# Kernel optimization log

Hardware: AMD Instinct MI355X
Metric: run time of the kernel (lower is better)

The kernel has to match this reference:

```python
import jax, jax.numpy as jnp
import numpy as np

N_NODES = 50000
N_EDGES = 800000
N_GRAPHS = 8
D_IN, D_HID, D_OUT = 128, 128, 64


def setup_inputs() -> dict:
    key = jax.random.key(0)
    ks = jax.random.split(key, 8)
    x = jax.random.normal(ks[0], (N_NODES, D_IN), jnp.float32)
    src = jax.random.randint(ks[1], (N_EDGES,), 0, N_NODES, dtype=jnp.int32)
    dst = jax.random.randint(ks[2], (N_EDGES,), 0, N_NODES, dtype=jnp.int32)
    graph_id = jnp.sort(jax.random.randint(ks[3], (N_NODES,), 0, N_GRAPHS, dtype=jnp.int32))
    s1 = 1.0 / np.sqrt(D_IN)
    s2 = 1.0 / np.sqrt(D_HID)
    W1 = jax.random.normal(ks[4], (D_IN, D_HID), jnp.float32) * s1
    b1 = jnp.zeros((D_HID,), jnp.float32)
    W2 = jax.random.normal(ks[5], (D_HID, D_HID), jnp.float32) * s2
    b2 = jnp.zeros((D_HID,), jnp.float32)
    Wl = jax.random.normal(ks[6], (D_HID, D_OUT), jnp.float32) * s2
    bl = jnp.zeros((D_OUT,), jnp.float32)
    return dict(x=x, W1=W1, b1=b1, W2=W2, b2=b2, Wl=Wl, bl=bl,
                src=src, dst=dst, graph_id=graph_id)


def _graph_conv(x, W, b, src, dst):
    # DGL GraphConv, norm='both': h' = D_in^{-1/2} A (D_out^{-1/2} x W) + b
    n = x.shape[0]
    ones = jnp.ones((src.shape[0],), x.dtype)
    out_deg = jax.ops.segment_sum(ones, src, num_segments=n)
    in_deg = jax.ops.segment_sum(ones, dst, num_segments=n)
    norm_src = jax.lax.rsqrt(jnp.clip(out_deg, 1.0))  # [N]
    norm_dst = jax.lax.rsqrt(jnp.clip(in_deg, 1.0))   # [N]
    h = (x * norm_src[:, None]) @ W                    # [N, D]
    agg = jax.ops.segment_sum(h[src], dst, num_segments=n)  # gather-scatter SpMM
    return agg * norm_dst[:, None] + b


def reference(x, W1, b1, W2, b2, Wl, bl, src, dst, graph_id):
    h = jax.nn.relu(_graph_conv(x, W1, b1, src, dst))
    h = _graph_conv(h, W2, b2, src, dst)
    # dgl.mean_nodes over batched graph: per-graph mean of node features
    cnt = jax.ops.segment_sum(jnp.ones((x.shape[0],), x.dtype), graph_id,
                              num_segments=N_GRAPHS)
    pooled = jax.ops.segment_sum(h, graph_id, num_segments=N_GRAPHS)
    means = pooled / jnp.clip(cnt, 1.0)[:, None]       # [B, D_HID]
    return means @ Wl + bl                              # [B, D_OUT]
```

## Files before the change

### kernel.cpp

```cpp
#include <hip/hip_runtime.h>
#include <hip/hip_bf16.h>

#define N_NODES 50000
#define N_EDGES 800000
#define N_GRAPHS 8
#define MAXDEG 64
#define NRANGE 4
#define NCHUNK 64
#define RSZ (N_NODES / NRANGE)
#define CHE (N_EDGES / NCHUNK)

typedef __attribute__((ext_vector_type(8))) short short8;
typedef __attribute__((ext_vector_type(4))) float floatx4;
typedef __attribute__((ext_vector_type(2))) float floatx2;

static __device__ __forceinline__ ushort f2b(float f) {
    union { float f; unsigned u; } v; v.f = f;
    return (ushort)((v.u + 0x7FFF + ((v.u >> 16) & 1)) >> 16);
}
static __device__ __forceinline__ float b2f(unsigned u) {
    union { unsigned u; float f; } v; v.u = u << 16;
    return v.f;
}
static __device__ __forceinline__ unsigned char f2q(float f) {
    int p = __builtin_amdgcn_cvt_pk_fp8_f32(f, f, 0, false);
    return (unsigned char)(p & 0xff);
}

__global__ __launch_bounds__(1024) void prep_kernel(
    const int* __restrict__ src, const int* __restrict__ dst,
    const float* __restrict__ W1, const float* __restrict__ W2,
    const int* __restrict__ gid,
    ushort* __restrict__ counts_in, ushort* __restrict__ counts_out,
    ushort* __restrict__ Wt1, ushort* __restrict__ Wt2,
    int* __restrict__ start)
{
    int b = blockIdx.x, t = threadIdx.x;
    if (b < 256) {
        __shared__ unsigned h[RSZ];
        int c = b & (NCHUNK - 1), r = b >> 6;
        int lo = r * RSZ;
        for (int j = t; j < RSZ; j += 1024) h[j] = 0;
        __syncthreads();
        int ebeg = c * CHE, eend = ebeg + CHE;
        for (int i = ebeg + t; i < eend; i += 1024) {
            int s = src[i], d = dst[i];
            unsigned ds = (unsigned)(d - lo);
            if (ds < RSZ) atomicAdd(&h[ds >> 1], 1u << ((ds & 1) * 16));
            unsigned ss = (unsigned)(s - lo);
            if (ss < RSZ) atomicAdd(&h[(RSZ / 2) + (ss >> 1)], 1u << ((ss & 1) * 16));
        }
        __syncthreads();
        unsigned* ci = (unsigned*)(counts_in  + (size_t)c * N_NODES + lo);
        unsigned* co = (unsigned*)(counts_out + (size_t)c * N_NODES + lo);
        for (int j = t; j < RSZ / 2; j += 1024) {
            ci[j] = h[j];
            co[j] = h[(RSZ / 2) + j];
        }
    } else if (b < 272) {
        int i = (b - 256) * 1024 + t;
        int c = i >> 7, k = i & 127;
        Wt1[i] = f2b(W1[k * 128 + c]);
        Wt2[i] = f2b(W2[k * 128 + c]);
    } else {
        int i = (b - 272) * 1024 + t;
        if (i < N_NODES) {
            int g = gid[i];
            int gp = (i == 0) ? -1 : gid[i - 1];
            for (int k = gp + 1; k <= g; ++k) start[k] = i;
            if (i == N_NODES - 1)
                for (int k = g + 1; k <= N_GRAPHS; ++k) start[k] = N_NODES;
        }
    }
}

__global__ __launch_bounds__(256) void scan_kernel(
    const ushort* __restrict__ counts_in, const ushort* __restrict__ counts_out,
    ushort* __restrict__ base, int* __restrict__ in_deg,
    float* __restrict__ ns, float* __restrict__ nd)
{
    int v = blockIdx.x * 256 + threadIdx.x;
    if (v >= N_NODES) return;
    unsigned od = 0;
    #pragma unroll 8
    for (int c = 0; c < NCHUNK; ++c) od += counts_out[(size_t)c * N_NODES + v];
    unsigned run = 0;
    #pragma unroll 8
    for (int c = 0; c < NCHUNK; ++c) {
        base[(size_t)c * N_NODES + v] = (ushort)run;
        run += counts_in[(size_t)c * N_NODES + v];
    }
    in_deg[v] = (int)run;
    ns[v] = rsqrtf(fmaxf((float)od, 1.f));
    nd[v] = rsqrtf(fmaxf((float)run, 1.f));
}

__global__ __launch_bounds__(1024) void scatter_kernel(
    const int* __restrict__ src, const int* __restrict__ dst,
    const ushort* __restrict__ base, ushort* __restrict__ slot)
{
    __shared__ unsigned h[RSZ / 2];
    int t = threadIdx.x;
    int c = blockIdx.x & (NCHUNK - 1), r = blockIdx.x >> 6;
    int lo = r * RSZ;
    const unsigned* bp = (const unsigned*)(base + (size_t)c * N_NODES + lo);
    for (int j = t; j < RSZ / 2; j += 1024) h[j] = bp[j];
    __syncthreads();
    int ebeg = c * CHE, eend = ebeg + CHE;
    for (int i = ebeg + t; i < eend; i += 1024) {
        int d = dst[i];
        unsigned ds = (unsigned)(d - lo);
        if (ds < RSZ) {
            int sh = (ds & 1) * 16;
            unsigned old = atomicAdd(&h[ds >> 1], 1u << sh);
            unsigned pos = (old >> sh) & 0xffff;
            if (pos < MAXDEG) slot[(size_t)d * MAXDEG + pos] = (ushort)src[i];
        }
    }
}

template<int FP32_IN>
__global__ __launch_bounds__(256, 2) void mfma_gemm_kernel(
    const void* __restrict__ Xv, const float* __restrict__ scale,
    const ushort* __restrict__ Wt, unsigned char* __restrict__ Y, int n)
{
    int t = threadIdx.x;
    int wv = t >> 6, lane = t & 63;
    int m = lane & 15, q = lane >> 4;
    short8 B[8][4];
    #pragma unroll
    for (int cb = 0; cb < 8; ++cb)
        #pragma unroll
        for (int kb = 0; kb < 4; ++kb)
            B[cb][kb] = *(const short8*)&Wt[(size_t)(cb * 16 + m) * 128 + kb * 32 + q * 8];

    int ntile = n >> 4;
    int gw = blockIdx.x * 4 + wv;
    for (int tile = gw; tile < ntile; tile += 2048) {
        int row = tile * 16 + m;
        short8 a[4];
        if (FP32_IN) {
            const float* X = (const float*)Xv;
            float s = scale[row];
            #pragma unroll
            for (int kb = 0; kb < 4; ++kb) {
                const float* p = X + (size_t)row * 128 + kb * 32 + q * 8;
                float4 f0 = *(const float4*)p;
                float4 f1 = *(const float4*)(p + 4);
                short8 av;
                av[0] = (short)f2b(f0.x * s); av[1] = (short)f2b(f0.y * s);
                av[2] = (short)f2b(f0.z * s); av[3] = (short)f2b(f0.w * s);
                av[4] = (short)f2b(f1.x * s); av[5] = (short)f2b(f1.y * s);
                av[6] = (short)f2b(f1.z * s); av[7] = (short)f2b(f1.w * s);
                a[kb] = av;
            }
        } else {
            const ushort* X = (const ushort*)Xv;
            #pragma unroll
            for (int kb = 0; kb < 4; ++kb)
                a[kb] = *(const short8*)(X + (size_t)row * 128 + kb * 32 + q * 8);
        }
        floatx4 acc[8] = {};
        #pragma unroll
        for (int cb = 0; cb < 8; ++cb)
            #pragma unroll
            for (int kb = 0; kb < 4; ++kb)
                acc[cb] = __builtin_amdgcn_mfma_f32_16x16x32_bf16(a[kb], B[cb][kb], acc[cb], 0, 0, 0);
        int rowbase = tile * 16 + q * 4;
        #pragma unroll
        for (int cb = 0; cb < 8; ++cb)
            #pragma unroll
            for (int r = 0; r < 4; ++r)
                Y[(size_t)(rowbase + r) * 128 + cb * 16 + m] = f2q(acc[cb][r]);
    }
}

__global__ __launch_bounds__(256) void spmm_fp8_kernel(
    const unsigned char* __restrict__ H, const int* __restrict__ in_deg,
    const ushort* __restrict__ slot, const float* __restrict__ norm_dst,
    const float* __restrict__ norm_src, const float* __restrict__ bias,
    ushort* __restrict__ Y, int n, int relu_scale)
{
    int w = (blockIdx.x * blockDim.x + threadIdx.x) >> 6;
    int lane = threadIdx.x & 63;
    if (w >= n) return;
    int cnt = min(in_deg[w], MAXDEG);
    const ushort* lst = slot + (size_t)w * MAXDEG;
    int g = lane >> 4;
    int c8 = (lane & 15) * 8;
    int myslot = lst[lane];
    float acc[8] = {};
    for (int e = 0; e < cnt; e += 4) {
        int idx = e + g;
        bool ok = idx < cnt;
        int s = __shfl(myslot, ok ? idx : 0, 64);
        if (ok) {
            uint2 v = *(const uint2*)&H[(size_t)s * 128 + c8];
            floatx2 p01 = __builtin_amdgcn_cvt_pk_f32_fp8((int)v.x, false);
            floatx2 p23 = __builtin_amdgcn_cvt_pk_f32_fp8((int)v.x, true);
            floatx2 p45 = __builtin_amdgcn_cvt_pk_f32_fp8((int)v.y, false);
            floatx2 p67 = __builtin_amdgcn_cvt_pk_f32_fp8((int)v.y, true);
            acc[0] += p01.x; acc[1] += p01.y;
            acc[2] += p23.x; acc[3] += p23.y;
            acc[4] += p45.x; acc[5] += p45.y;
            acc[6] += p67.x; acc[7] += p67.y;
        }
    }
    #pragma unroll
    for (int j = 0; j < 8; ++j) {
        acc[j] += __shfl_xor(acc[j], 16, 64);
        acc[j] += __shfl_xor(acc[j], 32, 64);
    }
    float ndv = norm_dst[w];
    float4 b0 = *(const float4*)&bias[c8];
    float4 b1 = *(const float4*)&bias[c8 + 4];
    float r[8];
    r[0] = acc[0] * ndv + b0.x; r[1] = acc[1] * ndv + b0.y;
    r[2] = acc[2] * ndv + b0.z; r[3] = acc[3] * ndv + b0.w;
    r[4] = acc[4] * ndv + b1.x; r[5] = acc[5] * ndv + b1.y;
    r[6] = acc[6] * ndv + b1.z; r[7] = acc[7] * ndv + b1.w;
    if (relu_scale) {
        float nsv = norm_src[w];
        #pragma unroll
        for (int j = 0; j < 8; ++j) r[j] = fmaxf(r[j], 0.f) * nsv;
    }
    if (lane < 16) {
        uint4 o;
        o.x = (unsigned)f2b(r[0]) | ((unsigned)f2b(r[1]) << 16);
        o.y = (unsigned)f2b(r[2]) | ((unsigned)f2b(r[3]) << 16);
        o.z = (unsigned)f2b(r[4]) | ((unsigned)f2b(r[5]) << 16);
        o.w = (unsigned)f2b(r[6]) | ((unsigned)f2b(r[7]) << 16);
        *(uint4*)&Y[(size_t)w * 128 + c8] = o;
    }
}

__global__ __launch_bounds__(256) void pool_kernel(
    const ushort* __restrict__ H, const int* __restrict__ start,
    float* __restrict__ part)
{
    __shared__ float red[128];
    int t = threadIdx.x;
    int g = blockIdx.x >> 5, j = blockIdx.x & 31;
    int beg0 = start[g], len = start[g + 1] - beg0;
    int sbeg = beg0 + (int)(((long long)len * j) >> 5);
    int send = beg0 + (int)(((long long)len * (j + 1)) >> 5);
    int wv = t >> 6, lane = t & 63;
    int rg = lane >> 4;
    int c8 = (lane & 15) * 8;
    float acc[8] = {};
    for (int v = sbeg + wv * 4 + rg; v < send; v += 16) {
        uint4 u = *(const uint4*)&H[(size_t)v * 128 + c8];
        acc[0] += b2f(u.x & 0xffff); acc[1] += b2f(u.x >> 16);
        acc[2] += b2f(u.y & 0xffff); acc[3] += b2f(u.y >> 16);
        acc[4] += b2f(u.z & 0xffff); acc[5] += b2f(u.z >> 16);
        acc[6] += b2f(u.w & 0xffff); acc[7] += b2f(u.w >> 16);
    }
    #pragma unroll
    for (int k = 0; k < 8; ++k) {
        acc[k] += __shfl_xor(acc[k], 16, 64);
        acc[k] += __shfl_xor(acc[k], 32, 64);
    }
    if (t < 128) red[t] = 0.f;
    __syncthreads();
    if (lane < 16) {
        #pragma unroll
        for (int k = 0; k < 8; ++k) atomicAdd(&red[c8 + k], acc[k]);
    }
    __syncthreads();
    if (t < 128) part[(size_t)blockIdx.x * 128 + t] = red[t];
}

__global__ __launch_bounds__(512) void head_kernel(
    const float* __restrict__ part, const int* __restrict__ start,
    const float* __restrict__ Wl, const float* __restrict__ bl,
    float* __restrict__ out)
{
    __shared__ float means[N_GRAPHS * 128];
    int t = threadIdx.x;
    for (int i = t; i < N_GRAPHS * 128; i += 512) {
        int g = i >> 7, k = i & 127;
        float s = 0.f;
        #pragma unroll 8
        for (int j = 0; j < 32; ++j) s += part[(size_t)(g * 32 + j) * 128 + k];
        float cnt = (float)(start[g + 1] - start[g]);
        means[i] = s / fmaxf(cnt, 1.f);
    }
    __syncthreads();
    int g = t >> 6, c = t & 63;
    float acc = bl[c];
    #pragma unroll 8
    for (int k = 0; k < 128; ++k)
        acc = fmaf(means[g * 128 + k], Wl[k * 64 + c], acc);
    out[g * 64 + c] = acc;
}

extern "C" void kernel_launch(void* const* d_in, const int* in_sizes, int n_in,
                              void* d_out, int out_size, void* d_ws, size_t ws_size,
                              hipStream_t stream) {
    const float* x   = (const float*)d_in[0];
    const float* W1  = (const float*)d_in[1];
    const float* b1  = (const float*)d_in[2];
    const float* W2  = (const float*)d_in[3];
    const float* b2  = (const float*)d_in[4];
    const float* Wl  = (const float*)d_in[5];
    const float* bl  = (const float*)d_in[6];
    const int*   src = (const int*)d_in[7];
    const int*   dst = (const int*)d_in[8];
    const int*   gid = (const int*)d_in[9];

    const int n = N_NODES;

    char* ws = (char*)d_ws;
    size_t off = 0;
    auto alloc = [&](size_t bytes) { size_t o = off; off += (bytes + 255) & ~(size_t)255; return o; };
    unsigned char* hA = (unsigned char*)(ws + alloc((size_t)n * 128));
    ushort* hB        = (ushort*)(ws + alloc((size_t)n * 128 * 2));
    ushort* slot      = (ushort*)(ws + alloc((size_t)n * MAXDEG * 2));
    ushort* counts_in = (ushort*)(ws + alloc((size_t)NCHUNK * n * 2));
    ushort* counts_out= (ushort*)(ws + alloc((size_t)NCHUNK * n * 2));
    ushort* basev     = (ushort*)(ws + alloc((size_t)NCHUNK * n * 2));
    float* norm_src   = (float*) (ws + alloc((size_t)n * 4));
    float* norm_dst   = (float*) (ws + alloc((size_t)n * 4));
    int*   in_deg     = (int*)   (ws + alloc((size_t)n * 4));
    int*   startb     = (int*)   (ws + alloc((size_t)(N_GRAPHS + 1) * 4));
    ushort* Wt1       = (ushort*)(ws + alloc((size_t)128 * 128 * 2));
    ushort* Wt2       = (ushort*)(ws + alloc((size_t)128 * 128 * 2));
    float* part       = (float*) (ws + alloc((size_t)N_GRAPHS * 32 * 128 * 4));

    int spmm_blocks = (n + 3) / 4;

    prep_kernel<<<321, 1024, 0, stream>>>(src, dst, W1, W2, gid,
                                          counts_in, counts_out, Wt1, Wt2, startb);
    scan_kernel<<<(n + 255) / 256, 256, 0, stream>>>(counts_in, counts_out, basev,
                                                     in_deg, norm_src, norm_dst);
    scatter_kernel<<<NRANGE * NCHUNK, 1024, 0, stream>>>(src, dst, basev, slot);
    mfma_gemm_kernel<1><<<512, 256, 0, stream>>>(x, norm_src, Wt1, hA, n);
    spmm_fp8_kernel<<<spmm_blocks, 256, 0, stream>>>(hA, in_deg, slot, norm_dst,
                                                     norm_src, b1, hB, n, 1);
    mfma_gemm_kernel<0><<<512, 256, 0, stream>>>(hB, nullptr, Wt2, hA, n);
    spmm_fp8_kernel<<<spmm_blocks, 256, 0, stream>>>(hA, in_deg, slot, norm_dst,
                                                     nullptr, b2, hB, n, 0);
    pool_kernel<<<N_GRAPHS * 32, 256, 0, stream>>>(hB, startb, part);
    head_kernel<<<1, 512, 0, stream>>>(part, startb, Wl, bl, (float*)d_out);
}
```

Measured before the change: 213.4 us.

## Replace chunked LDS histogram/scan/scatter with global atomic slot build

Removes the three-kernel degree count, prefix scan and chunked scatter, replacing them with a single kernel that uses global atomics on per-node in/out counters to both count degrees and place edges into fixed-width slots. The normalization factors are now computed on the fly from the counters in the GEMM and SpMM kernels, and the GEMM launches one tile per wave with swapped MFMA operands so each lane writes four packed fp8 bytes at once. This trades two launches and large intermediate count arrays for contended global atomics, and makes the order of neighbors within a slot list nondeterministic.

New measurement: 268.9 us. +26.0%, slower.

```diff
diff --git a/kernel.cpp b/kernel.cpp
--- a/kernel.cpp
+++ b/kernel.cpp
@@ -5,10 +5,6 @@
 #define N_EDGES 800000
 #define N_GRAPHS 8
 #define MAXDEG 64
-#define NRANGE 4
-#define NCHUNK 64
-#define RSZ (N_NODES / NRANGE)
-#define CHE (N_EDGES / NCHUNK)
 
 typedef __attribute__((ext_vector_type(8))) short short8;
 typedef __attribute__((ext_vector_type(4))) float floatx4;
@@ -22,48 +18,21 @@
     union { unsigned u; float f; } v; v.u = u << 16;
     return v.f;
 }
-static __device__ __forceinline__ unsigned char f2q(float f) {
-    int p = __builtin_amdgcn_cvt_pk_fp8_f32(f, f, 0, false);
-    return (unsigned char)(p & 0xff);
-}
-
-__global__ __launch_bounds__(1024) void prep_kernel(
-    const int* __restrict__ src, const int* __restrict__ dst,
+
+__global__ __launch_bounds__(1024) void prep0_kernel(
     const float* __restrict__ W1, const float* __restrict__ W2,
-    const int* __restrict__ gid,
-    ushort* __restrict__ counts_in, ushort* __restrict__ counts_out,
+    const int* __restrict__ gid, unsigned* __restrict__ curs,
     ushort* __restrict__ Wt1, ushort* __restrict__ Wt2,
     int* __restrict__ start)
 {
     int b = blockIdx.x, t = threadIdx.x;
-    if (b < 256) {
-        __shared__ unsigned h[RSZ];
-        int c = b & (NCHUNK - 1), r = b >> 6;
-        int lo = r * RSZ;
-        for (int j = t; j < RSZ; j += 1024) h[j] = 0;
-        __syncthreads();
-        int ebeg = c * CHE, eend = ebeg + CHE;
-        for (int i = ebeg + t; i < eend; i += 1024) {
-            int s = src[i], d = dst[i];
-            unsigned ds = (unsigned)(d - lo);
-            if (ds < RSZ) atomicAdd(&h[ds >> 1], 1u << ((ds & 1) * 16));
-            unsigned ss = (unsigned)(s - lo);
-            if (ss < RSZ) atomicAdd(&h[(RSZ / 2) + (ss >> 1)], 1u << ((ss & 1) * 16));
-        }
-        __syncthreads();
-        unsigned* ci = (unsigned*)(counts_in  + (size_t)c * N_NODES + lo);
-        unsigned* co = (unsigned*)(counts_out + (size_t)c * N_NODES + lo);
-        for (int j = t; j < RSZ / 2; j += 1024) {
-            ci[j] = h[j];
-            co[j] = h[(RSZ / 2) + j];
-        }
-    } else if (b < 272) {
-        int i = (b - 256) * 1024 + t;
+    if (b < 16) {
+        int i = b * 1024 + t;
         int c = i >> 7, k = i & 127;
         Wt1[i] = f2b(W1[k * 128 + c]);
         Wt2[i] = f2b(W2[k * 128 + c]);
-    } else {
-        int i = (b - 272) * 1024 + t;
+    } else if (b < 65) {
+        int i = (b - 16) * 1024 + t;
         if (i < N_NODES) {
             int g = gid[i];
             int gp = (i == 0) ? -1 : gid[i - 1];
@@ -71,62 +40,35 @@
             if (i == N_NODES - 1)
                 for (int k = g + 1; k <= N_GRAPHS; ++k) start[k] = N_NODES;
         }
-    }
-}
-
-__global__ __launch_bounds__(256) void scan_kernel(
-    const ushort* __restrict__ counts_in, const ushort* __restrict__ counts_out,
-    ushort* __restrict__ base, int* __restrict__ in_deg,
-    float* __restrict__ ns, float* __restrict__ nd)
-{
-    int v = blockIdx.x * 256 + threadIdx.x;
-    if (v >= N_NODES) return;
-    unsigned od = 0;
-    #pragma unroll 8
-    for (int c = 0; c < NCHUNK; ++c) od += counts_out[(size_t)c * N_NODES + v];
-    unsigned run = 0;
-    #pragma unroll 8
-    for (int c = 0; c < NCHUNK; ++c) {
-        base[(size_t)c * N_NODES + v] = (ushort)run;
-        run += counts_in[(size_t)c * N_NODES + v];
-    }
-    in_deg[v] = (int)run;
-    ns[v] = rsqrtf(fmaxf((float)od, 1.f));
-    nd[v] = rsqrtf(fmaxf((float)run, 1.f));
-}
-
-__global__ __launch_bounds__(1024) void scatter_kernel(
+    } else {
+        int i = (b - 65) * 1024 + t;
+        if (i < (2 * N_NODES) / 4) ((uint4*)curs)[i] = make_uint4(0, 0, 0, 0);
+    }
+}
+
+__global__ __launch_bounds__(256) void edge_scatter_kernel(
     const int* __restrict__ src, const int* __restrict__ dst,
-    const ushort* __restrict__ base, ushort* __restrict__ slot)
-{
-    __shared__ unsigned h[RSZ / 2];
-    int t = threadIdx.x;
-    int c = blockIdx.x & (NCHUNK - 1), r = blockIdx.x >> 6;
-    int lo = r * RSZ;
-    const unsigned* bp = (const unsigned*)(base + (size_t)c * N_NODES + lo);
-    for (int j = t; j < RSZ / 2; j += 1024) h[j] = bp[j];
-    __syncthreads();
-    int ebeg = c * CHE, eend = ebeg + CHE;
-    for (int i = ebeg + t; i < eend; i += 1024) {
-        int d = dst[i];
-        unsigned ds = (unsigned)(d - lo);
-        if (ds < RSZ) {
-            int sh = (ds & 1) * 16;
-            unsigned old = atomicAdd(&h[ds >> 1], 1u << sh);
-            unsigned pos = (old >> sh) & 0xffff;
-            if (pos < MAXDEG) slot[(size_t)d * MAXDEG + pos] = (ushort)src[i];
-        }
-    }
+    unsigned* __restrict__ in_cur, unsigned* __restrict__ out_cur,
+    ushort* __restrict__ slot)
+{
+    int i = blockIdx.x * 256 + threadIdx.x;
+    int s = src[i], d = dst[i];
+    atomicAdd(&out_cur[s], 1u);
+    unsigned pos = atomicAdd(&in_cur[d], 1u);
+    if (pos < MAXDEG) slot[(size_t)d * MAXDEG + pos] = (ushort)s;
 }
 
 template<int FP32_IN>
 __global__ __launch_bounds__(256, 2) void mfma_gemm_kernel(
-    const void* __restrict__ Xv, const float* __restrict__ scale,
-    const ushort* __restrict__ Wt, unsigned char* __restrict__ Y, int n)
+    const void* __restrict__ Xv, const unsigned* __restrict__ odeg,
+    const ushort* __restrict__ Wt, unsigned char* __restrict__ Y)
 {
     int t = threadIdx.x;
     int wv = t >> 6, lane = t & 63;
     int m = lane & 15, q = lane >> 4;
+    int tile = blockIdx.x * 4 + wv;
+    if (tile >= (N_NODES >> 4)) return;
+
     short8 B[8][4];
     #pragma unroll
     for (int cb = 0; cb < 8; ++cb)
@@ -134,57 +76,55 @@
         for (int kb = 0; kb < 4; ++kb)
             B[cb][kb] = *(const short8*)&Wt[(size_t)(cb * 16 + m) * 128 + kb * 32 + q * 8];
 
-    int ntile = n >> 4;
-    int gw = blockIdx.x * 4 + wv;
-    for (int tile = gw; tile < ntile; tile += 2048) {
-        int row = tile * 16 + m;
-        short8 a[4];
-        if (FP32_IN) {
-            const float* X = (const float*)Xv;
-            float s = scale[row];
-            #pragma unroll
-            for (int kb = 0; kb < 4; ++kb) {
-                const float* p = X + (size_t)row * 128 + kb * 32 + q * 8;
-                float4 f0 = *(const float4*)p;
-                float4 f1 = *(const float4*)(p + 4);
-                short8 av;
-                av[0] = (short)f2b(f0.x * s); av[1] = (short)f2b(f0.y * s);
-                av[2] = (short)f2b(f0.z * s); av[3] = (short)f2b(f0.w * s);
-                av[4] = (short)f2b(f1.x * s); av[5] = (short)f2b(f1.y * s);
-                av[6] = (short)f2b(f1.z * s); av[7] = (short)f2b(f1.w * s);
-                a[kb] = av;
-            }
-        } else {
-            const ushort* X = (const ushort*)Xv;
-            #pragma unroll
-            for (int kb = 0; kb < 4; ++kb)
-                a[kb] = *(const short8*)(X + (size_t)row * 128 + kb * 32 + q * 8);
+    int row = tile * 16 + m;
+    short8 a[4];
+    if (FP32_IN) {
+        const float* X = (const float*)Xv;
+        float s = rsqrtf(fmaxf((float)odeg[row], 1.f));
+        #pragma unroll
+        for (int kb = 0; kb < 4; ++kb) {
+            const float* p = X + (size_t)row * 128 + kb * 32 + q * 8;
+            float4 f0 = *(const float4*)p;
+            float4 f1 = *(const float4*)(p + 4);
+            short8 av;
+            av[0] = (short)f2b(f0.x * s); av[1] = (short)f2b(f0.y * s);
+            av[2] = (short)f2b(f0.z * s); av[3] = (short)f2b(f0.w * s);
+            av[4] = (short)f2b(f1.x * s); av[5] = (short)f2b(f1.y * s);
+            av[6] = (short)f2b(f1.z * s); av[7] = (short)f2b(f1.w * s);
+            a[kb] = av;
         }
-        floatx4 acc[8] = {};
-        #pragma unroll
-        for (int cb = 0; cb < 8; ++cb)
-            #pragma unroll
-            for (int kb = 0; kb < 4; ++kb)
-                acc[cb] = __builtin_amdgcn_mfma_f32_16x16x32_bf16(a[kb], B[cb][kb], acc[cb], 0, 0, 0);
-        int rowbase = tile * 16 + q * 4;
-        #pragma unroll
-        for (int cb = 0; cb < 8; ++cb)
-            #pragma unroll
-            for (int r = 0; r < 4; ++r)
-                Y[(size_t)(rowbase + r) * 128 + cb * 16 + m] = f2q(acc[cb][r]);
+    } else {
+        const ushort* X = (const ushort*)Xv;
+        #pragma unroll
+        for (int kb = 0; kb < 4; ++kb)
+            a[kb] = *(const short8*)(X + (size_t)row * 128 + kb * 32 + q * 8);
+    }
+    floatx4 acc[8] = {};
+    #pragma unroll
+    for (int cb = 0; cb < 8; ++cb)
+        #pragma unroll
+        for (int kb = 0; kb < 4; ++kb)
+            acc[cb] = __builtin_amdgcn_mfma_f32_16x16x32_bf16(B[cb][kb], a[kb], acc[cb], 0, 0, 0);
+
+    unsigned char* yr = Y + (size_t)row * 128;
+    #pragma unroll
+    for (int cb = 0; cb < 8; ++cb) {
+        int lo = __builtin_amdgcn_cvt_pk_fp8_f32(acc[cb][0], acc[cb][1], 0, false);
+        int pk = __builtin_amdgcn_cvt_pk_fp8_f32(acc[cb][2], acc[cb][3], lo, true);
+        *(unsigned*)(yr + cb * 16 + q * 4) = (unsigned)pk;
     }
 }
 
 __global__ __launch_bounds__(256) void spmm_fp8_kernel(
-    const unsigned char* __restrict__ H, const int* __restrict__ in_deg,
-    const ushort* __restrict__ slot, const float* __restrict__ norm_dst,
-    const float* __restrict__ norm_src, const float* __restrict__ bias,
-    ushort* __restrict__ Y, int n, int relu_scale)
+    const unsigned char* __restrict__ H, const unsigned* __restrict__ in_cur,
+    const unsigned* __restrict__ out_cur, const ushort* __restrict__ slot,
+    const float* __restrict__ bias, ushort* __restrict__ Y, int relu_scale)
 {
     int w = (blockIdx.x * blockDim.x + threadIdx.x) >> 6;
     int lane = threadIdx.x & 63;
-    if (w >= n) return;
-    int cnt = min(in_deg[w], MAXDEG);
+    if (w >= N_NODES) return;
+    int dg = (int)in_cur[w];
+    int cnt = min(dg, MAXDEG);
     const ushort* lst = slot + (size_t)w * MAXDEG;
     int g = lane >> 4;
     int c8 = (lane & 15) * 8;
@@ -211,7 +151,7 @@
         acc[j] += __shfl_xor(acc[j], 16, 64);
         acc[j] += __shfl_xor(acc[j], 32, 64);
     }
-    float ndv = norm_dst[w];
+    float ndv = rsqrtf(fmaxf((float)dg, 1.f));
     float4 b0 = *(const float4*)&bias[c8];
     float4 b1 = *(const float4*)&bias[c8 + 4];
     float r[8];
@@ -220,7 +160,7 @@
     r[4] = acc[4] * ndv + b1.x; r[5] = acc[5] * ndv + b1.y;
     r[6] = acc[6] * ndv + b1.z; r[7] = acc[7] * ndv + b1.w;
     if (relu_scale) {
-        float nsv = norm_src[w];
+        float nsv = rsqrtf(fmaxf((float)out_cur[w], 1.f));
         #pragma unroll
         for (int j = 0; j < 8; ++j) r[j] = fmaxf(r[j], 0.f) * nsv;
     }
@@ -316,30 +256,24 @@
     unsigned char* hA = (unsigned char*)(ws + alloc((size_t)n * 128));
     ushort* hB        = (ushort*)(ws + alloc((size_t)n * 128 * 2));
     ushort* slot      = (ushort*)(ws + alloc((size_t)n * MAXDEG * 2));
-    ushort* counts_in = (ushort*)(ws + alloc((size_t)NCHUNK * n * 2));
-    ushort* counts_out= (ushort*)(ws + alloc((size_t)NCHUNK * n * 2));
-    ushort* basev     = (ushort*)(ws + alloc((size_t)NCHUNK * n * 2));
-    float* norm_src   = (float*) (ws + alloc((size_t)n * 4));
-    float* norm_dst   = (float*) (ws + alloc((size_t)n * 4));
-    int*   in_deg     = (int*)   (ws + alloc((size_t)n * 4));
+    unsigned* curs    = (unsigned*)(ws + alloc((size_t)2 * n * 4));
     int*   startb     = (int*)   (ws + alloc((size_t)(N_GRAPHS + 1) * 4));
     ushort* Wt1       = (ushort*)(ws + alloc((size_t)128 * 128 * 2));
     ushort* Wt2       = (ushort*)(ws + alloc((size_t)128 * 128 * 2));
     float* part       = (float*) (ws + alloc((size_t)N_GRAPHS * 32 * 128 * 4));
 
+    unsigned* in_cur  = curs;
+    unsigned* out_cur = curs + n;
+
     int spmm_blocks = (n + 3) / 4;
-
-    prep_kernel<<<321, 1024, 0, stream>>>(src, dst, W1, W2, gid,
-                                          counts_in, counts_out, Wt1, Wt2, startb);
-    scan_kernel<<<(n + 255) / 256, 256, 0, stream>>>(counts_in, counts_out, basev,
-                                                     in_deg, norm_src, norm_dst);
-    scatter_kernel<<<NRANGE * NCHUNK, 1024, 0, stream>>>(src, dst, basev, slot);
-    mfma_gemm_kernel<1><<<512, 256, 0, stream>>>(x, norm_src, Wt1, hA, n);
-    spmm_fp8_kernel<<<spmm_blocks, 256, 0, stream>>>(hA, in_deg, slot, norm_dst,
-                                                     norm_src, b1, hB, n, 1);
-    mfma_gemm_kernel<0><<<512, 256, 0, stream>>>(hB, nullptr, Wt2, hA, n);
-    spmm_fp8_kernel<<<spmm_blocks, 256, 0, stream>>>(hA, in_deg, slot, norm_dst,
-                                                     nullptr, b2, hB, n, 0);
+    int gemm_blocks = ((n >> 4) + 3) / 4;
+
+    prep0_kernel<<<90, 1024, 0, stream>>>(W1, W2, gid, curs, Wt1, Wt2, startb);
+    edge_scatter_kernel<<<N_EDGES / 256, 256, 0, stream>>>(src, dst, in_cur, out_cur, slot);
+    mfma_gemm_kernel<1><<<gemm_blocks, 256, 0, stream>>>(x, out_cur, Wt1, hA);
+    spmm_fp8_kernel<<<spmm_blocks, 256, 0, stream>>>(hA, in_cur, out_cur, slot, b1, hB, 1);
+    mfma_gemm_kernel<0><<<gemm_blocks, 256, 0, stream>>>(hB, out_cur, Wt2, hA);
+    spmm_fp8_kernel<<<spmm_blocks, 256, 0, stream>>>(hA, in_cur, out_cur, slot, b2, hB, 0);
     pool_kernel<<<N_GRAPHS * 32, 256, 0, stream>>>(hB, startb, part);
     head_kernel<<<1, 512, 0, stream>>>(part, startb, Wl, bl, (float*)d_out);
 }
```

## Pad neighbor lists with zero sentinel row, unroll SpMM, transpose MFMA for packed stores

Applied to the files above, without the earlier changes.

Neighbor slot lists are pre-filled with 0xFFFF, and a zeroed sentinel row 65535 is added to the hA buffer. The SpMM loop can then process 8 edges per iteration without bounds checks, since padded slots read zeros. The GEMM swaps its MFMA operands so each lane holds four consecutive output columns and writes them as one packed 4-byte fp8 store. It also launches one wave per tile instead of using a grid-stride loop. The cost is an extra 6.4 MB slot fill in the prep kernel and wasted loads on padded edges.

Measured after the change: 218.6 us. 2.4% more time.

```diff
diff --git a/kernel.cpp b/kernel.cpp
--- a/kernel.cpp
+++ b/kernel.cpp
@@ -9,6 +9,7 @@
 #define NCHUNK 64
 #define RSZ (N_NODES / NRANGE)
 #define CHE (N_EDGES / NCHUNK)
+#define SENT_ROW 65535
 
 typedef __attribute__((ext_vector_type(8))) short short8;
 typedef __attribute__((ext_vector_type(4))) float floatx4;
@@ -33,7 +34,8 @@
     const int* __restrict__ gid,
     ushort* __restrict__ counts_in, ushort* __restrict__ counts_out,
     ushort* __restrict__ Wt1, ushort* __restrict__ Wt2,
-    int* __restrict__ start)
+    int* __restrict__ start,
+    unsigned char* __restrict__ hA, uint4* __restrict__ slot_fill)
 {
     int b = blockIdx.x, t = threadIdx.x;
     if (b < 256) {
@@ -62,7 +64,9 @@
         int c = i >> 7, k = i & 127;
         Wt1[i] = f2b(W1[k * 128 + c]);
         Wt2[i] = f2b(W2[k * 128 + c]);
-    } else {
+        if (b == 256 && t < 32)
+            ((unsigned*)(hA + (size_t)SENT_ROW * 128))[t] = 0u;
+    } else if (b < 321) {
         int i = (b - 272) * 1024 + t;
         if (i < N_NODES) {
             int g = gid[i];
@@ -71,6 +75,10 @@
             if (i == N_NODES - 1)
                 for (int k = g + 1; k <= N_GRAPHS; ++k) start[k] = N_NODES;
         }
+    } else {
+        int i = (b - 321) * 1024 + t;
+        if (i < (N_NODES * MAXDEG * 2) / 16)
+            slot_fill[i] = make_uint4(0xFFFFFFFFu, 0xFFFFFFFFu, 0xFFFFFFFFu, 0xFFFFFFFFu);
     }
 }
 
@@ -122,11 +130,14 @@
 template<int FP32_IN>
 __global__ __launch_bounds__(256, 2) void mfma_gemm_kernel(
     const void* __restrict__ Xv, const float* __restrict__ scale,
-    const ushort* __restrict__ Wt, unsigned char* __restrict__ Y, int n)
+    const ushort* __restrict__ Wt, unsigned char* __restrict__ Y)
 {
     int t = threadIdx.x;
     int wv = t >> 6, lane = t & 63;
     int m = lane & 15, q = lane >> 4;
+    int tile = blockIdx.x * 4 + wv;
+    if (tile >= (N_NODES >> 4)) return;
+
     short8 B[8][4];
     #pragma unroll
     for (int cb = 0; cb < 8; ++cb)
@@ -134,44 +145,42 @@
         for (int kb = 0; kb < 4; ++kb)
             B[cb][kb] = *(const short8*)&Wt[(size_t)(cb * 16 + m) * 128 + kb * 32 + q * 8];
 
-    int ntile = n >> 4;
-    int gw = blockIdx.x * 4 + wv;
-    for (int tile = gw; tile < ntile; tile += 2048) {
-        int row = tile * 16 + m;
-        short8 a[4];
-        if (FP32_IN) {
-            const float* X = (const float*)Xv;
-            float s = scale[row];
-            #pragma unroll
-            for (int kb = 0; kb < 4; ++kb) {
-                const float* p = X + (size_t)row * 128 + kb * 32 + q * 8;
-                float4 f0 = *(const float4*)p;
-                float4 f1 = *(const float4*)(p + 4);
-                short8 av;
-                av[0] = (short)f2b(f0.x * s); av[1] = (short)f2b(f0.y * s);
-                av[2] = (short)f2b(f0.z * s); av[3] = (short)f2b(f0.w * s);
-                av[4] = (short)f2b(f1.x * s); av[5] = (short)f2b(f1.y * s);
-                av[6] = (short)f2b(f1.z * s); av[7] = (short)f2b(f1.w * s);
-                a[kb] = av;
-            }
-        } else {
-            const ushort* X = (const ushort*)Xv;
-            #pragma unroll
-            for (int kb = 0; kb < 4; ++kb)
-                a[kb] = *(const short8*)(X + (size_t)row * 128 + kb * 32 + q * 8);
-        }
-        floatx4 acc[8] = {};
-        #pragma unroll
-        for (int cb = 0; cb < 8; ++cb)
-            #pragma unroll
-            for (int kb = 0; kb < 4; ++kb)
-                acc[cb] = __builtin_amdgcn_mfma_f32_16x16x32_bf16(a[kb], B[cb][kb], acc[cb], 0, 0, 0);
-        int rowbase = tile * 16 + q * 4;
-        #pragma unroll
-        for (int cb = 0; cb < 8; ++cb)
-            #pragma unroll
-            for (int r = 0; r < 4; ++r)
-                Y[(size_t)(rowbase + r) * 128 + cb * 16 + m] = f2q(acc[cb][r]);
+    int row = tile * 16 + m;
+    short8 a[4];
+    if (FP32_IN) {
+        const float* X = (const float*)Xv;
+        float s = scale[row];
+        #pragma unroll
+        for (int kb = 0; kb < 4; ++kb) {
+            const float* p = X + (size_t)row * 128 + kb * 32 + q * 8;
+            float4 f0 = *(const float4*)p;
+            float4 f1 = *(const float4*)(p + 4);
+            short8 av;
+            av[0] = (short)f2b(f0.x * s); av[1] = (short)f2b(f0.y * s);
+            av[2] = (short)f2b(f0.z * s); av[3] = (short)f2b(f0.w * s);
+            av[4] = (short)f2b(f1.x * s); av[5] = (short)f2b(f1.y * s);
+            av[6] = (short)f2b(f1.z * s); av[7] = (short)f2b(f1.w * s);
+            a[kb] = av;
+        }
+    } else {
+        const ushort* X = (const ushort*)Xv;
+        #pragma unroll
+        for (int kb = 0; kb < 4; ++kb)
+            a[kb] = *(const short8*)(X + (size_t)row * 128 + kb * 32 + q * 8);
+    }
+    floatx4 acc[8] = {};
+    #pragma unroll
+    for (int cb = 0; cb < 8; ++cb)
+        #pragma unroll
+        for (int kb = 0; kb < 4; ++kb)
+            acc[cb] = __builtin_amdgcn_mfma_f32_16x16x32_bf16(B[cb][kb], a[kb], acc[cb], 0, 0, 0);
+
+    unsigned char* yr = Y + (size_t)row * 128;
+    #pragma unroll
+    for (int cb = 0; cb < 8; ++cb) {
+        int lo = __builtin_amdgcn_cvt_pk_fp8_f32(acc[cb][0], acc[cb][1], 0, false);
+        int pk = __builtin_amdgcn_cvt_pk_fp8_f32(acc[cb][2], acc[cb][3], lo, true);
+        *(unsigned*)(yr + cb * 16 + q * 4) = (unsigned)pk;
     }
 }
 
@@ -179,32 +188,34 @@
     const unsigned char* __restrict__ H, const int* __restrict__ in_deg,
     const ushort* __restrict__ slot, const float* __restrict__ norm_dst,
     const float* __restrict__ norm_src, const float* __restrict__ bias,
-    ushort* __restrict__ Y, int n, int relu_scale)
+    ushort* __restrict__ Y, int relu_scale)
 {
     int w = (blockIdx.x * blockDim.x + threadIdx.x) >> 6;
     int lane = threadIdx.x & 63;
-    if (w >= n) return;
+    if (w >= N_NODES) return;
     int cnt = min(in_deg[w], MAXDEG);
     const ushort* lst = slot + (size_t)w * MAXDEG;
     int g = lane >> 4;
     int c8 = (lane & 15) * 8;
     int myslot = lst[lane];
     float acc[8] = {};
-    for (int e = 0; e < cnt; e += 4) {
-        int idx = e + g;
-        bool ok = idx < cnt;
-        int s = __shfl(myslot, ok ? idx : 0, 64);
-        if (ok) {
-            uint2 v = *(const uint2*)&H[(size_t)s * 128 + c8];
-            floatx2 p01 = __builtin_amdgcn_cvt_pk_f32_fp8((int)v.x, false);
-            floatx2 p23 = __builtin_amdgcn_cvt_pk_f32_fp8((int)v.x, true);
-            floatx2 p45 = __builtin_amdgcn_cvt_pk_f32_fp8((int)v.y, false);
-            floatx2 p67 = __builtin_amdgcn_cvt_pk_f32_fp8((int)v.y, true);
-            acc[0] += p01.x; acc[1] += p01.y;
-            acc[2] += p23.x; acc[3] += p23.y;
-            acc[4] += p45.x; acc[5] += p45.y;
-            acc[6] += p67.x; acc[7] += p67.y;
-        }
+    for (int e = 0; e < cnt; e += 8) {
+        int s0 = __shfl(myslot, e + g, 64);
+        int s1 = __shfl(myslot, e + 4 + g, 64);
+        uint2 v0 = *(const uint2*)&H[(size_t)s0 * 128 + c8];
+        uint2 v1 = *(const uint2*)&H[(size_t)s1 * 128 + c8];
+        floatx2 a01 = __builtin_amdgcn_cvt_pk_f32_fp8((int)v0.x, false);
+        floatx2 a23 = __builtin_amdgcn_cvt_pk_f32_fp8((int)v0.x, true);
+        floatx2 a45 = __builtin_amdgcn_cvt_pk_f32_fp8((int)v0.y, false);
+        floatx2 a67 = __builtin_amdgcn_cvt_pk_f32_fp8((int)v0.y, true);
+        floatx2 b01 = __builtin_amdgcn_cvt_pk_f32_fp8((int)v1.x, false);
+        floatx2 b23 = __builtin_amdgcn_cvt_pk_f32_fp8((int)v1.x, true);
+        floatx2 b45 = __builtin_amdgcn_cvt_pk_f32_fp8((int)v1.y, false);
+        floatx2 b67 = __builtin_amdgcn_cvt_pk_f32_fp8((int)v1.y, true);
+        acc[0] += a01.x + b01.x; acc[1] += a01.y + b01.y;
+        acc[2] += a23.x + b23.x; acc[3] += a23.y + b23.y;
+        acc[4] += a45.x + b45.x; acc[5] += a45.y + b45.y;
+        acc[6] += a67.x + b67.x; acc[7] += a67.y + b67.y;
     }
     #pragma unroll
     for (int j = 0; j < 8; ++j) {
@@ -313,7 +324,7 @@
     char* ws = (char*)d_ws;
     size_t off = 0;
     auto alloc = [&](size_t bytes) { size_t o = off; off += (bytes + 255) & ~(size_t)255; return o; };
-    unsigned char* hA = (unsigned char*)(ws + alloc((size_t)n * 128));
+    unsigned char* hA = (unsigned char*)(ws + alloc((size_t)65536 * 128));
     ushort* hB        = (ushort*)(ws + alloc((size_t)n * 128 * 2));
     ushort* slot      = (ushort*)(ws + alloc((size_t)n * MAXDEG * 2));
     ushort* counts_in = (ushort*)(ws + alloc((size_t)NCHUNK * n * 2));
@@ -328,18 +339,21 @@
     float* part       = (float*) (ws + alloc((size_t)N_GRAPHS * 32 * 128 * 4));
 
     int spmm_blocks = (n + 3) / 4;
-
-    prep_kernel<<<321, 1024, 0, stream>>>(src, dst, W1, W2, gid,
-                                          counts_in, counts_out, Wt1, Wt2, startb);
+    int gemm_blocks = ((n >> 4) + 3) / 4;
+    int fill_blocks = ((N_NODES * MAXDEG * 2) / 16 + 1023) / 1024;
+
+    prep_kernel<<<321 + fill_blocks, 1024, 0, stream>>>(
+        src, dst, W1, W2, gid, counts_in, counts_out, Wt1, Wt2, startb,
+        hA, (uint4*)slot);
     scan_kernel<<<(n + 255) / 256, 256, 0, stream>>>(counts_in, counts_out, basev,
                                                      in_deg, norm_src, norm_dst);
     scatter_kernel<<<NRANGE * NCHUNK, 1024, 0, stream>>>(src, dst, basev, slot);
-    mfma_gemm_kernel<1><<<512, 256, 0, stream>>>(x, norm_src, Wt1, hA, n);
+    mfma_gemm_kernel<1><<<gemm_blocks, 256, 0, stream>>>(x, norm_src, Wt1, hA);
     spmm_fp8_kernel<<<spmm_blocks, 256, 0, stream>>>(hA, in_deg, slot, norm_dst,
-                                                     norm_src, b1, hB, n, 1);
-    mfma_gemm_kernel<0><<<512, 256, 0, stream>>>(hB, nullptr, Wt2, hA, n);
+                                                     norm_src, b1, hB, 1);
+    mfma_gemm_kernel<0><<<gemm_blocks, 256, 0, stream>>>(hB, nullptr, Wt2, hA);
     spmm_fp8_kernel<<<spmm_blocks, 256, 0, stream>>>(hA, in_deg, slot, norm_dst,
-                                                     nullptr, b2, hB, n, 0);
+                                                     nullptr, b2, hB, 0);
     pool_kernel<<<N_GRAPHS * 32, 256, 0, stream>>>(hB, startb, part);
     head_kernel<<<1, 512, 0, stream>>>(part, startb, Wl, bl, (float*)d_out);
 }
```

## Transpose MFMA operands for packed fp8 stores and launch one tile per wave

Applied to the files above, without the earlier changes.

Swaps the A/B operands of the bf16 MFMA so each lane holds four consecutive output columns of one row. This lets the epilogue pack them into a single 32-bit fp8 store per column block instead of 32 scattered byte stores. The GEMM now launches one wave per 16-row tile rather than using a grid-stride loop over 512 blocks. The SpMM gains an occupancy hint of 8 blocks per CU, and n is replaced by the compile-time node count. The tradeoff is that every wave reloads the full weight fragment into registers, adding redundant weight loads.

New measurement: 228.6 us. +7.1%, slower.

```diff
diff --git a/kernel.cpp b/kernel.cpp
--- a/kernel.cpp
+++ b/kernel.cpp
@@ -21,10 +21,6 @@
 static __device__ __forceinline__ float b2f(unsigned u) {
     union { unsigned u; float f; } v; v.u = u << 16;
     return v.f;
-}
-static __device__ __forceinline__ unsigned char f2q(float f) {
-    int p = __builtin_amdgcn_cvt_pk_fp8_f32(f, f, 0, false);
-    return (unsigned char)(p & 0xff);
 }
 
 __global__ __launch_bounds__(1024) void prep_kernel(
@@ -122,11 +118,14 @@
 template<int FP32_IN>
 __global__ __launch_bounds__(256, 2) void mfma_gemm_kernel(
     const void* __restrict__ Xv, const float* __restrict__ scale,
-    const ushort* __restrict__ Wt, unsigned char* __restrict__ Y, int n)
+    const ushort* __restrict__ Wt, unsigned char* __restrict__ Y)
 {
     int t = threadIdx.x;
     int wv = t >> 6, lane = t & 63;
     int m = lane & 15, q = lane >> 4;
+    int tile = blockIdx.x * 4 + wv;
+    if (tile >= (N_NODES >> 4)) return;
+
     short8 B[8][4];
     #pragma unroll
     for (int cb = 0; cb < 8; ++cb)
@@ -134,56 +133,54 @@
         for (int kb = 0; kb < 4; ++kb)
             B[cb][kb] = *(const short8*)&Wt[(size_t)(cb * 16 + m) * 128 + kb * 32 + q * 8];
 
-    int ntile = n >> 4;
-    int gw = blockIdx.x * 4 + wv;
-    for (int tile = gw; tile < ntile; tile += 2048) {
-        int row = tile * 16 + m;
-        short8 a[4];
-        if (FP32_IN) {
-            const float* X = (const float*)Xv;
-            float s = scale[row];
-            #pragma unroll
-            for (int kb = 0; kb < 4; ++kb) {
-                const float* p = X + (size_t)row * 128 + kb * 32 + q * 8;
-                float4 f0 = *(const float4*)p;
-                float4 f1 = *(const float4*)(p + 4);
-                short8 av;
-                av[0] = (short)f2b(f0.x * s); av[1] = (short)f2b(f0.y * s);
-                av[2] = (short)f2b(f0.z * s); av[3] = (short)f2b(f0.w * s);
-                av[4] = (short)f2b(f1.x * s); av[5] = (short)f2b(f1.y * s);
-                av[6] = (short)f2b(f1.z * s); av[7] = (short)f2b(f1.w * s);
-                a[kb] = av;
-            }
-        } else {
-            const ushort* X = (const ushort*)Xv;
-            #pragma unroll
-            for (int kb = 0; kb < 4; ++kb)
-                a[kb] = *(const short8*)(X + (size_t)row * 128 + kb * 32 + q * 8);
-        }
-        floatx4 acc[8] = {};
-        #pragma unroll
-        for (int cb = 0; cb < 8; ++cb)
-            #pragma unroll
-            for (int kb = 0; kb < 4; ++kb)
-                acc[cb] = __builtin_amdgcn_mfma_f32_16x16x32_bf16(a[kb], B[cb][kb], acc[cb], 0, 0, 0);
-        int rowbase = tile * 16 + q * 4;
-        #pragma unroll
-        for (int cb = 0; cb < 8; ++cb)
-            #pragma unroll
-            for (int r = 0; r < 4; ++r)
-                Y[(size_t)(rowbase + r) * 128 + cb * 16 + m] = f2q(acc[cb][r]);
-    }
-}
-
-__global__ __launch_bounds__(256) void spmm_fp8_kernel(
+    int row = tile * 16 + m;
+    short8 a[4];
+    if (FP32_IN) {
+        const float* X = (const float*)Xv;
+        float s = scale[row];
+        #pragma unroll
+        for (int kb = 0; kb < 4; ++kb) {
+            const float* p = X + (size_t)row * 128 + kb * 32 + q * 8;
+            float4 f0 = *(const float4*)p;
+            float4 f1 = *(const float4*)(p + 4);
+            short8 av;
+            av[0] = (short)f2b(f0.x * s); av[1] = (short)f2b(f0.y * s);
+            av[2] = (short)f2b(f0.z * s); av[3] = (short)f2b(f0.w * s);
+            av[4] = (short)f2b(f1.x * s); av[5] = (short)f2b(f1.y * s);
+            av[6] = (short)f2b(f1.z * s); av[7] = (short)f2b(f1.w * s);
+            a[kb] = av;
+        }
+    } else {
+        const ushort* X = (const ushort*)Xv;
+        #pragma unroll
+        for (int kb = 0; kb < 4; ++kb)
+            a[kb] = *(const short8*)(X + (size_t)row * 128 + kb * 32 + q * 8);
+    }
+    floatx4 acc[8] = {};
+    #pragma unroll
+    for (int cb = 0; cb < 8; ++cb)
+        #pragma unroll
+        for (int kb = 0; kb < 4; ++kb)
+            acc[cb] = __builtin_amdgcn_mfma_f32_16x16x32_bf16(B[cb][kb], a[kb], acc[cb], 0, 0, 0);
+
+    unsigned char* yr = Y + (size_t)row * 128;
+    #pragma unroll
+    for (int cb = 0; cb < 8; ++cb) {
+        int lo = __builtin_amdgcn_cvt_pk_fp8_f32(acc[cb][0], acc[cb][1], 0, false);
+        int pk = __builtin_amdgcn_cvt_pk_fp8_f32(acc[cb][2], acc[cb][3], lo, true);
+        *(unsigned*)(yr + cb * 16 + q * 4) = (unsigned)pk;
+    }
+}
+
+__global__ __launch_bounds__(256, 8) void spmm_fp8_kernel(
     const unsigned char* __restrict__ H, const int* __restrict__ in_deg,
     const ushort* __restrict__ slot, const float* __restrict__ norm_dst,
     const float* __restrict__ norm_src, const float* __restrict__ bias,
-    ushort* __restrict__ Y, int n, int relu_scale)
+    ushort* __restrict__ Y, int relu_scale)
 {
     int w = (blockIdx.x * blockDim.x + threadIdx.x) >> 6;
     int lane = threadIdx.x & 63;
-    if (w >= n) return;
+    if (w >= N_NODES) return;
     int cnt = min(in_deg[w], MAXDEG);
     const ushort* lst = slot + (size_t)w * MAXDEG;
     int g = lane >> 4;
@@ -328,18 +325,19 @@
     float* part       = (float*) (ws + alloc((size_t)N_GRAPHS * 32 * 128 * 4));
 
     int spmm_blocks = (n + 3) / 4;
+    int gemm_blocks = ((n >> 4) + 3) / 4;
 
     prep_kernel<<<321, 1024, 0, stream>>>(src, dst, W1, W2, gid,
                                           counts_in, counts_out, Wt1, Wt2, startb);
     scan_kernel<<<(n + 255) / 256, 256, 0, stream>>>(counts_in, counts_out, basev,
                                                      in_deg, norm_src, norm_dst);
     scatter_kernel<<<NRANGE * NCHUNK, 1024, 0, stream>>>(src, dst, basev, slot);
-    mfma_gemm_kernel<1><<<512, 256, 0, stream>>>(x, norm_src, Wt1, hA, n);
+    mfma_gemm_kernel<1><<<gemm_blocks, 256, 0, stream>>>(x, norm_src, Wt1, hA);
     spmm_fp8_kernel<<<spmm_blocks, 256, 0, stream>>>(hA, in_deg, slot, norm_dst,
-                                                     norm_src, b1, hB, n, 1);
-    mfma_gemm_kernel<0><<<512, 256, 0, stream>>>(hB, nullptr, Wt2, hA, n);
+                                                     norm_src, b1, hB, 1);
+    mfma_gemm_kernel<0><<<gemm_blocks, 256, 0, stream>>>(hB, nullptr, Wt2, hA);
     spmm_fp8_kernel<<<spmm_blocks, 256, 0, stream>>>(hA, in_deg, slot, norm_dst,
-                                                     nullptr, b2, hB, n, 0);
+                                                     nullptr, b2, hB, 0);
     pool_kernel<<<N_GRAPHS * 32, 256, 0, stream>>>(hB, startb, part);
     head_kernel<<<1, 512, 0, stream>>>(part, startb, Wl, bl, (float*)d_out);
 }
```
